# Kernel optimization log

Measured on AMD Instinct MI355X. Metric: run time of the kernel, lower is better.

The kernel has to match this reference:

```python
import jax, jax.numpy as jnp
import numpy as np

HEADS = 4
DIM_HEAD = 32
EPS = 1e-5


def setup_inputs() -> dict:
    key = jax.random.key(0)
    ks = jax.random.split(key, 3)
    B, C, H, W = 4, 128, 64, 64
    hidden = HEADS * DIM_HEAD  # 128
    x = jax.random.normal(ks[0], (B, C, H, W), dtype=jnp.float32)
    g = jnp.ones((1, C, 1, 1), dtype=jnp.float32)
    b = jnp.zeros((1, C, 1, 1), dtype=jnp.float32)
    # 1x1 convs are channel matmuls; init like torch kaiming-uniform scale
    w_qkv = jax.random.normal(ks[1], (hidden * 3, C), dtype=jnp.float32) * (1.0 / np.sqrt(C))
    w_out = jax.random.normal(ks[2], (C, hidden), dtype=jnp.float32) * (1.0 / np.sqrt(hidden))
    b_out = jnp.zeros((C,), dtype=jnp.float32)
    return {"x": x, "g": g, "b": b, "w_qkv": w_qkv, "w_out": w_out, "b_out": b_out}


def reference(x, g, b, w_qkv, w_out, b_out):
    B, C, H, W = x.shape
    scale = DIM_HEAD ** -0.5
    # channel-wise LayerNorm (biased variance over channel dim)
    mean = jnp.mean(x, axis=1, keepdims=True)
    var = jnp.var(x, axis=1, keepdims=True)
    xn = (x - mean) / jnp.sqrt(var + EPS) * g + b
    # 1x1 conv qkv projection: [B, 3*hidden, H, W]
    qkv = jnp.einsum('oc,bchw->bohw', w_qkv, xn)
    hidden = HEADS * DIM_HEAD
    q, k, v = qkv[:, :hidden], qkv[:, hidden:2 * hidden], qkv[:, 2 * hidden:]
    # b (h d) x y -> b h d (x y)
    def split_heads(t):
        return t.reshape(B, HEADS, DIM_HEAD, H * W)
    q, k, v = split_heads(q) * scale, split_heads(k), split_heads(v)
    sim = jnp.einsum('bhdi,bhdj->bhij', q, k)            # [B, heads, HW, HW]
    attn = jax.nn.softmax(sim, axis=-1)
    out = jnp.einsum('bhij,bhdj->bhid', attn, v)          # [B, heads, HW, DIM_HEAD]
    # b h (x y) d -> b (h d) x y
    out = out.transpose(0, 1, 3, 2).reshape(B, hidden, H, W)
    return jnp.einsum('oc,bchw->bohw', w_out, out) + b_out[None, :, None, None]
```

## Files before the change

### kernel.cpp

```cpp
#include <hip/hip_runtime.h>
#include <math.h>

#define NPIX 4096
#define CCH  128

typedef __attribute__((ext_vector_type(8))) short  bf8;
typedef __attribute__((ext_vector_type(4))) float  f4;

typedef __attribute__((address_space(1))) const unsigned gu32;
typedef __attribute__((address_space(3))) unsigned       lu32;

#define MFMA(a, b, c) __builtin_amdgcn_mfma_f32_16x16x32_bf16(a, b, c, 0, 0, 0)

__device__ __forceinline__ unsigned short f2bf(float x) {
    union { float f; unsigned u; } v; v.f = x;
    unsigned r = v.u + 0x7fffu + ((v.u >> 16) & 1u);
    return (unsigned short)(r >> 16);
}
__device__ __forceinline__ unsigned pk2r(float lo, float hi) {
    union { float f; unsigned u; } a, b; a.f = hi; b.f = lo;
    return __builtin_amdgcn_perm(a.u + 0x8000u, b.u + 0x8000u, 0x07060302u);
}
__device__ __forceinline__ unsigned pk2t(float lo, float hi) {
    union { float f; unsigned u; } a, b; a.f = hi; b.f = lo;
    return __builtin_amdgcn_perm(a.u, b.u, 0x07060302u);
}


__global__ __launch_bounds__(256) void wconv_kernel(
    const float* __restrict__ wq, const float* __restrict__ wo,
    unsigned short* __restrict__ wqb, unsigned short* __restrict__ wob)
{
    const float qs2 = 0.17677669529663687f * 1.4426950408889634f;
    int i = blockIdx.x * 256 + threadIdx.x;
    if (i < 49152) {
        float f = wq[i];
        if (i < 16384) f *= qs2;
        wqb[i] = f2bf(f);
    } else {
        int j = i - 49152;
        wob[j] = f2bf(wo[j]);
    }
}

__global__ __launch_bounds__(256, 8) void lnqkv_kernel(
    const float* __restrict__ x, const float* __restrict__ g,
    const float* __restrict__ bvec, const unsigned short* __restrict__ wqb,
    unsigned short* __restrict__ qh, unsigned short* __restrict__ kh,
    unsigned short* __restrict__ vth)
{
    const int blk  = blockIdx.x;
    const int b  = blk >> 8;
    const int n0 = (blk & 255) << 4;
    const int t  = threadIdx.x;

    __shared__ float xs[CCH * 17];
    __shared__ float red0[16][16];
    __shared__ float red1[16][16];
    __shared__ float mean_s[16];
    __shared__ float rstd_s[16];
    __shared__ unsigned short xnb[16 * 138];

    const float* xb = x + (size_t)b * CCH * NPIX + n0;
#pragma unroll
    for (int k = 0; k < 8; ++k) {
        int e = k * 256 + t;
        int c = e >> 4, p = e & 15;
        xs[c * 17 + p] = xb[(size_t)c * NPIX + p];
    }
    __syncthreads();

    {
        int pix = t & 15, cg = t >> 4;
        float s = 0.f, s2 = 0.f;
#pragma unroll
        for (int cc = 0; cc < 8; ++cc) {
            float v = xs[(cg * 8 + cc) * 17 + pix];
            s += v; s2 += v * v;
        }
        red0[cg][pix] = s; red1[cg][pix] = s2;
    }
    __syncthreads();
    if (t < 16) {
        float s = 0.f, s2 = 0.f;
#pragma unroll
        for (int cg = 0; cg < 16; ++cg) { s += red0[cg][t]; s2 += red1[cg][t]; }
        float mu  = s * (1.f / 128.f);
        float var = s2 * (1.f / 128.f) - mu * mu;
        mean_s[t] = mu;
        rstd_s[t] = rsqrtf(var + 1e-5f);
    }
    __syncthreads();

    {
        const int pix = t >> 4;
        const int c0  = (t & 15) * 8;
        const float mu = mean_s[pix], rs = rstd_s[pix];
#pragma unroll
        for (int i = 0; i < 4; ++i) {
            int c = c0 + 2 * i;
            float f0 = (xs[c * 17 + pix]       - mu) * rs * g[c]     + bvec[c];
            float f1 = (xs[(c + 1) * 17 + pix] - mu) * rs * g[c + 1] + bvec[c + 1];
            *(unsigned*)&xnb[pix * 138 + c] = pk2r(f0, f1);
        }
    }
    __syncthreads();

    const int wv   = t >> 6;
    const int l16  = t & 15;
    const int quad = (t & 63) >> 4;

    for (int it = 0; it < 6; ++it) {
        const int ot = wv * 6 + it;
        const unsigned short* wr = wqb + (size_t)(ot * 16 + l16) * CCH;
        f4 acc = {0.f, 0.f, 0.f, 0.f};
#pragma unroll
        for (int kk = 0; kk < 4; ++kk) {
            const bf8 a = *(const bf8*)&wr[kk * 32 + quad * 8];
            const unsigned short* xr = &xnb[l16 * 138 + kk * 32 + quad * 8];
            union { unsigned u[4]; bf8 v; } bx;
            bx.u[0] = *(const unsigned*)&xr[0];
            bx.u[1] = *(const unsigned*)&xr[2];
            bx.u[2] = *(const unsigned*)&xr[4];
            bx.u[3] = *(const unsigned*)&xr[6];
            acc = MFMA(a, bx.v, acc);
        }
        if (ot < 16) {
            const int h  = (ot >> 1) & 3;
            const int d0 = (ot & 1) * 16 + quad * 4;
            const int bh = b * 4 + h;
            unsigned short* dst = ((ot < 8) ? qh : kh)
                                + ((size_t)bh * NPIX + n0 + l16) * 32 + d0;
            uint2 wp;
            wp.x = pk2r(acc.x, acc.y);
            wp.y = pk2r(acc.z, acc.w);
            *(uint2*)dst = wp;
        } else {
            const int bh = b * 4 + ((ot - 16) >> 1);
            const int dv = ((ot - 16) & 1) * 16 + quad * 4;
#pragma unroll
            for (int r = 0; r < 4; ++r)
                vth[((size_t)bh * 32 + dv + r) * NPIX + n0 + l16] = f2bf(acc[r]);
        }
    }
}

struct Frags { bf8 k0, k1, v0, v1; };

__device__ __forceinline__ void xpose(unsigned x0, unsigned y0,
                                      unsigned x1, unsigned y1,
                                      unsigned* u )
{
    auto sx = __builtin_amdgcn_permlane32_swap(x0, x1, false, false);
    auto sy = __builtin_amdgcn_permlane32_swap(y0, y1, false, false);
    auto dx = __builtin_amdgcn_permlane16_swap(sx[0], sx[1], false, false);
    auto dy = __builtin_amdgcn_permlane16_swap(sy[0], sy[1], false, false);
    u[0] = dx[0]; u[1] = dy[0]; u[2] = dx[1]; u[3] = dy[1];
}

__device__ __forceinline__ void tileCompute(const Frags& f,
    const bf8 qA, const bf8 qB, const bf8 ones,
    f4& o00, f4& o10, f4& o01, f4& o11, f4& lA, f4& lB)
{
    const f4 z = {0.f, 0.f, 0.f, 0.f};
    f4 sA0 = MFMA(f.k0, qA, z);
    f4 sA1 = MFMA(f.k1, qA, z);
    f4 sB0 = MFMA(f.k0, qB, z);
    f4 sB1 = MFMA(f.k1, qB, z);

    const unsigned a0x = pk2t(__builtin_amdgcn_exp2f(sA0.x), __builtin_amdgcn_exp2f(sA0.y));
    const unsigned a0y = pk2t(__builtin_amdgcn_exp2f(sA0.z), __builtin_amdgcn_exp2f(sA0.w));
    const unsigned a1x = pk2t(__builtin_amdgcn_exp2f(sA1.x), __builtin_amdgcn_exp2f(sA1.y));
    const unsigned a1y = pk2t(__builtin_amdgcn_exp2f(sA1.z), __builtin_amdgcn_exp2f(sA1.w));
    const unsigned b0x = pk2t(__builtin_amdgcn_exp2f(sB0.x), __builtin_amdgcn_exp2f(sB0.y));
    const unsigned b0y = pk2t(__builtin_amdgcn_exp2f(sB0.z), __builtin_amdgcn_exp2f(sB0.w));
    const unsigned b1x = pk2t(__builtin_amdgcn_exp2f(sB1.x), __builtin_amdgcn_exp2f(sB1.y));
    const unsigned b1y = pk2t(__builtin_amdgcn_exp2f(sB1.z), __builtin_amdgcn_exp2f(sB1.w));

    union { unsigned u[4]; bf8 v; } pA, pB;
    xpose(a0x, a0y, a1x, a1y, pA.u);
    xpose(b0x, b0y, b1x, b1y, pB.u);

    o00 = MFMA(f.v0, pA.v, o00); o10 = MFMA(f.v1, pA.v, o10);
    o01 = MFMA(f.v0, pB.v, o01); o11 = MFMA(f.v1, pB.v, o11);
    lA  = MFMA(ones, pA.v, lA);  lB  = MFMA(ones, pB.v, lB);
}

__global__ __launch_bounds__(256, 4) void flash_kernel(
    const unsigned short* __restrict__ qh, const unsigned short* __restrict__ kh,
    const unsigned short* __restrict__ vth,
    float* __restrict__ ao, float* __restrict__ lbuf)
{
    const int blk = blockIdx.x;
    const int bh  = (blk & 7) + 8 * ((blk >> 3) & 1);
    const int rem = blk >> 4;
    const int qt  = rem & 31;
    const int ks  = rem >> 5;
    const int t   = threadIdx.x;
    const int wv  = t >> 6;
    const int l16 = t & 15;
    const int quad = (t & 63) >> 4;
    const int q0  = qt * 128 + wv * 32;

    __shared__ __align__(16) unsigned short kv[2][2048];

    const size_t qbaseA = ((size_t)bh * NPIX + q0 + l16) * 32 + quad * 8;
    const bf8 qA = *(const bf8*)&qh[qbaseA];
    const bf8 qB = *(const bf8*)&qh[qbaseA + 16 * 32];

    const unsigned short* khb = kh  + (size_t)bh * NPIX * 32;
    const unsigned short* vhb = vth + (size_t)bh * 32 * NPIX;

    const int lane = t & 63;
    const int srow = lane >> 2;
    const int scol = (lane & 3) ^ ((lane >> 3) & 3);
    lu32* ldsbase[2];
    ldsbase[0] = (lu32*)&kv[0][wv * 512];
    ldsbase[1] = (lu32*)&kv[1][wv * 512];

    const short one = (short)0x3f80;
    const bf8 ones = {one, one, one, one, one, one, one, one};

    const f4 z = {0.f, 0.f, 0.f, 0.f};
    f4 o00 = z, o10 = z, o01 = z, o11 = z, lA = z, lB = z;

    const int jbase = ks * 2048;

#define STAGE(bufi, j0s)                                                        \
    {                                                                           \
        const unsigned short* gsrc = (wv < 2)                                   \
            ? khb + (size_t)((j0s) + wv * 16 + srow) * 32 + scol * 8            \
            : vhb + (size_t)((wv - 2) * 16 + srow) * NPIX + (j0s) + scol * 8;   \
        __builtin_amdgcn_global_load_lds((gu32*)gsrc, ldsbase[bufi], 16, 0, 0); \
    }

    STAGE(0, jbase);
    __syncthreads();

    const int sk = (quad ^ ((l16 >> 1) & 3)) * 8;
    for (int jt = 0; jt < 64; ++jt) {
        const int cur = jt & 1;
        if (jt < 63) STAGE(cur ^ 1, jbase + (jt + 1) * 32);
        const unsigned short* kb = kv[cur];
        Frags f;
        f.k0 = *(const bf8*)&kb[l16 * 32 + sk];
        f.k1 = *(const bf8*)&kb[(16 + l16) * 32 + sk];
        f.v0 = *(const bf8*)&kb[1024 + l16 * 32 + sk];
        f.v1 = *(const bf8*)&kb[1024 + (16 + l16) * 32 + sk];
        tileCompute(f, qA, qB, ones, o00, o10, o01, o11, lA, lB);
        __syncthreads();
    }
#undef STAGE

    float* aos = ao + (size_t)ks * 2097152;
    float* lbs = lbuf + (size_t)ks * 65536;
    float* aoA = aos + (size_t)bh * 32 * NPIX + q0 + l16;
    float* aoB = aoA + 16;
#pragma unroll
    for (int r = 0; r < 4; ++r) {
        aoA[(size_t)(quad * 4 + r) * NPIX]      = o00[r];
        aoA[(size_t)(16 + quad * 4 + r) * NPIX] = o10[r];
        aoB[(size_t)(quad * 4 + r) * NPIX]      = o01[r];
        aoB[(size_t)(16 + quad * 4 + r) * NPIX] = o11[r];
    }
    if (quad == 0) {
        lbs[(size_t)bh * NPIX + q0 + l16]      = lA.x;
        lbs[(size_t)bh * NPIX + q0 + 16 + l16] = lB.x;
    }
}

__global__ __launch_bounds__(256) void proj_kernel(
    const float* __restrict__ ao, const float* __restrict__ lbuf,
    const unsigned short* __restrict__ wob, const float* __restrict__ b_out,
    float* __restrict__ out)
{
    const int blk  = blockIdx.x;
    const int b  = blk >> 8;
    const int n0 = (blk & 255) << 4;
    const int t  = threadIdx.x;
    const int wv = t >> 6;
    const int l16 = t & 15;
    const int quad = (t & 63) >> 4;

    __shared__ unsigned short xsb[16 * 138];
    __shared__ float linv[4][16];

    if (t < 64) {
        int h = t >> 4, p = t & 15;
        size_t li = (size_t)(b * 4 + h) * NPIX + n0 + p;
        linv[h][p] = 1.0f / (lbuf[li] + lbuf[li + 65536]);
    }
    __syncthreads();

    const float* a0 = ao + (size_t)(b * CCH) * NPIX + n0;
    const float* a1 = a0 + 2097152;
#pragma unroll
    for (int k = 0; k < 2; ++k) {
        int idx = k * 256 + t;
        int c = idx >> 2, p4 = (idx & 3) * 4;
        const float4 va = *(const float4*)&a0[(size_t)c * NPIX + p4];
        const float4 vb = *(const float4*)&a1[(size_t)c * NPIX + p4];
        const int hh = c >> 5;
        xsb[(p4 + 0) * 138 + c] = f2bf((va.x + vb.x) * linv[hh][p4 + 0]);
        xsb[(p4 + 1) * 138 + c] = f2bf((va.y + vb.y) * linv[hh][p4 + 1]);
        xsb[(p4 + 2) * 138 + c] = f2bf((va.z + vb.z) * linv[hh][p4 + 2]);
        xsb[(p4 + 3) * 138 + c] = f2bf((va.w + vb.w) * linv[hh][p4 + 3]);
    }
    __syncthreads();

    bf8 pbf[4];
#pragma unroll
    for (int kk = 0; kk < 4; ++kk) {
        const unsigned short* row = &xsb[l16 * 138 + kk * 32 + quad * 8];
        union { unsigned u[4]; bf8 v; } pb;
        pb.u[0] = *(const unsigned*)&row[0];
        pb.u[1] = *(const unsigned*)&row[2];
        pb.u[2] = *(const unsigned*)&row[4];
        pb.u[3] = *(const unsigned*)&row[6];
        pbf[kk] = pb.v;
    }

    const f4 z = {0.f, 0.f, 0.f, 0.f};
#pragma unroll
    for (int p = 0; p < 2; ++p) {
        const int o0 = p * 64 + wv * 16;
        const unsigned short* wrow = wob + (size_t)(o0 + l16) * CCH;
        f4 acc = z;
#pragma unroll
        for (int kk = 0; kk < 4; ++kk) {
            const bf8 aw = *(const bf8*)&wrow[kk * 32 + quad * 8];
            acc = MFMA(aw, pbf[kk], acc);
        }
#pragma unroll
        for (int r = 0; r < 4; ++r) {
            const int o = o0 + quad * 4 + r;
            out[(size_t)(b * CCH + o) * NPIX + n0 + l16] = acc[r] + b_out[o];
        }
    }
}

extern "C" void kernel_launch(void* const* d_in, const int* in_sizes, int n_in,
                              void* d_out, int out_size, void* d_ws, size_t ws_size,
                              hipStream_t stream) {
    const float* x     = (const float*)d_in[0];
    const float* g     = (const float*)d_in[1];
    const float* bvec  = (const float*)d_in[2];
    const float* w_qkv = (const float*)d_in[3];
    const float* w_out = (const float*)d_in[4];
    const float* b_out = (const float*)d_in[5];
    float* out = (float*)d_out;

    char* ws = (char*)d_ws;
    float*          lbuf = (float*)(ws);
    unsigned short* wqb  = (unsigned short*)(ws + (1u << 20));
    unsigned short* wob  = (unsigned short*)(ws + (3u << 19));
    unsigned short* qh   = (unsigned short*)(ws + (4u  << 20));
    unsigned short* kh   = (unsigned short*)(ws + (8u  << 20));
    unsigned short* vth  = (unsigned short*)(ws + (12u << 20));
    float*          ao   = (float*)(ws + (16u << 20));

    wconv_kernel<<<dim3(256),  dim3(256), 0, stream>>>(w_qkv, w_out, wqb, wob);
    lnqkv_kernel<<<dim3(1024), dim3(256), 0, stream>>>(x, g, bvec, wqb, qh, kh, vth);
    flash_kernel<<<dim3(1024), dim3(256), 0, stream>>>(qh, kh, vth, ao, lbuf);
    proj_kernel <<<dim3(1024), dim3(256), 0, stream>>>(ao, lbuf, wob, b_out, out);
}
```

Measured before the change: 145.2 us.

## Split flash work to one 16-query tile per wave with 512-thread blocks

Each wave now handles 16 query rows instead of 32. The block grows to 8 waves so the same 128-query tile is covered, and only the first four waves stage K/V tiles into shared memory. This halves per-wave accumulator registers and doubles the number of waves sharing each staged K/V tile, aiming for more latency hiding. The cost is more waves reading the same LDS fragments and more barrier participants per tile.

New measurement: 145.6 us. Within noise of the previous version (+0.2%).

```diff
diff --git a/kernel.cpp b/kernel.cpp
--- a/kernel.cpp
+++ b/kernel.cpp
@@ -158,35 +158,28 @@
     u[0] = dx[0]; u[1] = dy[0]; u[2] = dx[1]; u[3] = dy[1];
 }
 
-__device__ __forceinline__ void tileCompute(const Frags& f,
-    const bf8 qA, const bf8 qB, const bf8 ones,
-    f4& o00, f4& o10, f4& o01, f4& o11, f4& lA, f4& lB)
+__device__ __forceinline__ void tileComputeA(const Frags& f,
+    const bf8 qA, const bf8 ones,
+    f4& o00, f4& o10, f4& lA)
 {
     const f4 z = {0.f, 0.f, 0.f, 0.f};
     f4 sA0 = MFMA(f.k0, qA, z);
     f4 sA1 = MFMA(f.k1, qA, z);
-    f4 sB0 = MFMA(f.k0, qB, z);
-    f4 sB1 = MFMA(f.k1, qB, z);
 
     const unsigned a0x = pk2t(__builtin_amdgcn_exp2f(sA0.x), __builtin_amdgcn_exp2f(sA0.y));
     const unsigned a0y = pk2t(__builtin_amdgcn_exp2f(sA0.z), __builtin_amdgcn_exp2f(sA0.w));
     const unsigned a1x = pk2t(__builtin_amdgcn_exp2f(sA1.x), __builtin_amdgcn_exp2f(sA1.y));
     const unsigned a1y = pk2t(__builtin_amdgcn_exp2f(sA1.z), __builtin_amdgcn_exp2f(sA1.w));
-    const unsigned b0x = pk2t(__builtin_amdgcn_exp2f(sB0.x), __builtin_amdgcn_exp2f(sB0.y));
-    const unsigned b0y = pk2t(__builtin_amdgcn_exp2f(sB0.z), __builtin_amdgcn_exp2f(sB0.w));
-    const unsigned b1x = pk2t(__builtin_amdgcn_exp2f(sB1.x), __builtin_amdgcn_exp2f(sB1.y));
-    const unsigned b1y = pk2t(__builtin_amdgcn_exp2f(sB1.z), __builtin_amdgcn_exp2f(sB1.w));
-
-    union { unsigned u[4]; bf8 v; } pA, pB;
+
+    union { unsigned u[4]; bf8 v; } pA;
     xpose(a0x, a0y, a1x, a1y, pA.u);
-    xpose(b0x, b0y, b1x, b1y, pB.u);
-
-    o00 = MFMA(f.v0, pA.v, o00); o10 = MFMA(f.v1, pA.v, o10);
-    o01 = MFMA(f.v0, pB.v, o01); o11 = MFMA(f.v1, pB.v, o11);
-    lA  = MFMA(ones, pA.v, lA);  lB  = MFMA(ones, pB.v, lB);
-}
-
-__global__ __launch_bounds__(256, 4) void flash_kernel(
+
+    o00 = MFMA(f.v0, pA.v, o00);
+    o10 = MFMA(f.v1, pA.v, o10);
+    lA  = MFMA(ones, pA.v, lA);
+}
+
+__global__ __launch_bounds__(512, 8) void flash_kernel(
     const unsigned short* __restrict__ qh, const unsigned short* __restrict__ kh,
     const unsigned short* __restrict__ vth,
     float* __restrict__ ao, float* __restrict__ lbuf)
@@ -200,13 +193,12 @@
     const int wv  = t >> 6;
     const int l16 = t & 15;
     const int quad = (t & 63) >> 4;
-    const int q0  = qt * 128 + wv * 32;
+    const int q0  = qt * 128 + wv * 16;
 
     __shared__ __align__(16) unsigned short kv[2][2048];
 
     const size_t qbaseA = ((size_t)bh * NPIX + q0 + l16) * 32 + quad * 8;
     const bf8 qA = *(const bf8*)&qh[qbaseA];
-    const bf8 qB = *(const bf8*)&qh[qbaseA + 16 * 32];
 
     const unsigned short* khb = kh  + (size_t)bh * NPIX * 32;
     const unsigned short* vhb = vth + (size_t)bh * 32 * NPIX;
@@ -214,20 +206,21 @@
     const int lane = t & 63;
     const int srow = lane >> 2;
     const int scol = (lane & 3) ^ ((lane >> 3) & 3);
+    const int wchunk = (wv & 3) * 512;
     lu32* ldsbase[2];
-    ldsbase[0] = (lu32*)&kv[0][wv * 512];
-    ldsbase[1] = (lu32*)&kv[1][wv * 512];
+    ldsbase[0] = (lu32*)&kv[0][wchunk];
+    ldsbase[1] = (lu32*)&kv[1][wchunk];
 
     const short one = (short)0x3f80;
     const bf8 ones = {one, one, one, one, one, one, one, one};
 
     const f4 z = {0.f, 0.f, 0.f, 0.f};
-    f4 o00 = z, o10 = z, o01 = z, o11 = z, lA = z, lB = z;
+    f4 o00 = z, o10 = z, lA = z;
 
     const int jbase = ks * 2048;
 
 #define STAGE(bufi, j0s)                                                        \
-    {                                                                           \
+    if (wv < 4) {                                                               \
         const unsigned short* gsrc = (wv < 2)                                   \
             ? khb + (size_t)((j0s) + wv * 16 + srow) * 32 + scol * 8            \
             : vhb + (size_t)((wv - 2) * 16 + srow) * NPIX + (j0s) + scol * 8;   \
@@ -247,7 +240,7 @@
         f.k1 = *(const bf8*)&kb[(16 + l16) * 32 + sk];
         f.v0 = *(const bf8*)&kb[1024 + l16 * 32 + sk];
         f.v1 = *(const bf8*)&kb[1024 + (16 + l16) * 32 + sk];
-        tileCompute(f, qA, qB, ones, o00, o10, o01, o11, lA, lB);
+        tileComputeA(f, qA, ones, o00, o10, lA);
         __syncthreads();
     }
 #undef STAGE
@@ -255,17 +248,13 @@
     float* aos = ao + (size_t)ks * 2097152;
     float* lbs = lbuf + (size_t)ks * 65536;
     float* aoA = aos + (size_t)bh * 32 * NPIX + q0 + l16;
-    float* aoB = aoA + 16;
 #pragma unroll
     for (int r = 0; r < 4; ++r) {
         aoA[(size_t)(quad * 4 + r) * NPIX]      = o00[r];
         aoA[(size_t)(16 + quad * 4 + r) * NPIX] = o10[r];
-        aoB[(size_t)(quad * 4 + r) * NPIX]      = o01[r];
-        aoB[(size_t)(16 + quad * 4 + r) * NPIX] = o11[r];
     }
     if (quad == 0) {
-        lbs[(size_t)bh * NPIX + q0 + l16]      = lA.x;
-        lbs[(size_t)bh * NPIX + q0 + 16 + l16] = lB.x;
+        lbs[(size_t)bh * NPIX + q0 + l16] = lA.x;
     }
 }
 
@@ -361,6 +350,6 @@
 
     wconv_kernel<<<dim3(256),  dim3(256), 0, stream>>>(w_qkv, w_out, wqb, wob);
     lnqkv_kernel<<<dim3(1024), dim3(256), 0, stream>>>(x, g, bvec, wqb, qh, kh, vth);
-    flash_kernel<<<dim3(1024), dim3(256), 0, stream>>>(qh, kh, vth, ao, lbuf);
+    flash_kernel<<<dim3(1024), dim3(512), 0, stream>>>(qh, kh, vth, ao, lbuf);
     proj_kernel <<<dim3(1024), dim3(256), 0, stream>>>(ao, lbuf, wob, b_out, out);
 }
```
